# Kernel tuning notes

Measured on AMD Instinct MI355X. Metric: run time of the kernel, lower is better.

## Reference

```python
import jax, jax.numpy as jnp
import numpy as np

N_NODES = 100000
N_EDGES = 1600000
NFEAT, NHID, NCLASS = 512, 128, 40


def setup_inputs() -> dict:
    key = jax.random.key(0)
    ks = jax.random.split(key, 8)
    features = jax.random.normal(ks[0], (N_NODES, NFEAT), dtype=jnp.float32)
    edge_src = jax.random.randint(ks[1], (N_EDGES,), 0, N_NODES, dtype=jnp.int32)
    edge_dst = jax.random.randint(ks[2], (N_EDGES,), 0, N_NODES, dtype=jnp.int32)
    edge_weight = jax.random.uniform(ks[3], (N_EDGES,), dtype=jnp.float32)
    W1 = jax.random.normal(ks[4], (NFEAT, NHID), dtype=jnp.float32) * (1.0 / np.sqrt(NFEAT))
    b1 = jnp.zeros((NHID,), dtype=jnp.float32)
    W2 = jax.random.normal(ks[5], (NHID, NCLASS), dtype=jnp.float32) * (1.0 / np.sqrt(NHID))
    b2 = jnp.zeros((NCLASS,), dtype=jnp.float32)
    return {"features": features, "edge_src": edge_src, "edge_dst": edge_dst,
            "edge_weight": edge_weight, "W1": W1, "b1": b1, "W2": W2, "b2": b2}


def _gcn_conv(x, W, b, edge_src, edge_dst, edge_weight, num_nodes):
    # GCNconv: adj @ (x @ W) + b, adj given as weighted edge list (spmm).
    h = x @ W                                   # [N, out]
    msgs = edge_weight[:, None] * h[edge_src]   # [E, out] gather + scale
    agg = jax.ops.segment_sum(msgs, edge_dst, num_segments=num_nodes)  # [N, out]
    return agg + b


def reference(features, edge_src, edge_dst, edge_weight, W1, b1, W2, b2):
    x = _gcn_conv(features, W1, b1, edge_src, edge_dst, edge_weight, N_NODES)
    x = jax.nn.relu(x)
    # dropout is identity in eval mode (deterministic reference)
    x = _gcn_conv(x, W2, b2, edge_src, edge_dst, edge_weight, N_NODES)
    return jax.nn.log_softmax(x, axis=1)
```

## Files before the change

### kernel.cpp

```cpp
#include <hip/hip_runtime.h>
#include <hip/hip_bf16.h>
#include <math.h>

#define N_NODES 100000
#define N_EDGES 1600000
#define NFEAT 512
#define NHID 128
#define NCLASS 40

#define SCAN_TILE 1024
#define SCAN_NB ((N_NODES + SCAN_TILE - 1) / SCAN_TILE)

#define BSH 8
#define BNODES (1 << BSH)
#define NBUCK ((N_NODES + BNODES - 1) / BNODES)

#define PCHUNK 4096
#define PEPT 16
#define PNB ((N_EDGES + PCHUNK - 1) / PCHUNK)

typedef short bf16x8 __attribute__((ext_vector_type(8)));
typedef float f32x4 __attribute__((ext_vector_type(4)));

static __device__ __forceinline__ unsigned short f32_to_bf16(float f) {
    unsigned int u = __float_as_uint(f);
    unsigned int r = u + 0x7FFFu + ((u >> 16) & 1u);
    return (unsigned short)(r >> 16);
}
static __device__ __forceinline__ float bf16_to_f32(unsigned short h) {
    return __uint_as_float(((unsigned int)h) << 16);
}

__global__ __launch_bounds__(256) void transpose_w1_kernel(
    const float* __restrict__ W1, unsigned short* __restrict__ Wt)
{
    int tid = blockIdx.x * 256 + threadIdx.x;
    int n = tid >> 9;
    int k = tid & 511;
    Wt[tid] = f32_to_bf16(W1[k * NHID + n]);
}

__global__ __launch_bounds__(256) void gemm1_mfma_kernel(
    const float* __restrict__ A,
    const unsigned short* __restrict__ Wt,
    unsigned short* __restrict__ h1b,
    int M)
{
    __shared__ unsigned short cstage[4][32 * 130];

    const int tid = threadIdx.x;
    const int w = tid >> 6;
    const int lane = tid & 63;
    const int lr = lane & 15;
    const int quad = lane >> 4;
    const int m0 = blockIdx.x * 128 + w * 32;

    f32x4 acc[2][8];
    #pragma unroll
    for (int rt = 0; rt < 2; rt++)
        #pragma unroll
        for (int ct = 0; ct < 8; ct++)
            acc[rt][ct] = (f32x4){0.f, 0.f, 0.f, 0.f};

    int r0 = m0 + lr;
    int r1 = m0 + 16 + lr;
    int r0c = r0 < M ? r0 : M - 1;
    int r1c = r1 < M ? r1 : M - 1;
    const float* a0p = A + (size_t)r0c * NFEAT + quad * 8;
    const float* a1p = A + (size_t)r1c * NFEAT + quad * 8;
    const unsigned short* bp = Wt + (size_t)lr * NFEAT + quad * 8;

    #pragma unroll 2
    for (int k0 = 0; k0 < NFEAT; k0 += 32) {
        float4 a0a = *(const float4*)(a0p + k0);
        float4 a0b = *(const float4*)(a0p + k0 + 4);
        float4 a1a = *(const float4*)(a1p + k0);
        float4 a1b = *(const float4*)(a1p + k0 + 4);

        bf16x8 fb[8];
        #pragma unroll
        for (int ct = 0; ct < 8; ct++)
            fb[ct] = *(const bf16x8*)(bp + (size_t)ct * 16 * NFEAT + k0);

        bf16x8 fa0, fa1;
        fa0[0] = (short)f32_to_bf16(a0a.x); fa0[1] = (short)f32_to_bf16(a0a.y);
        fa0[2] = (short)f32_to_bf16(a0a.z); fa0[3] = (short)f32_to_bf16(a0a.w);
        fa0[4] = (short)f32_to_bf16(a0b.x); fa0[5] = (short)f32_to_bf16(a0b.y);
        fa0[6] = (short)f32_to_bf16(a0b.z); fa0[7] = (short)f32_to_bf16(a0b.w);
        fa1[0] = (short)f32_to_bf16(a1a.x); fa1[1] = (short)f32_to_bf16(a1a.y);
        fa1[2] = (short)f32_to_bf16(a1a.z); fa1[3] = (short)f32_to_bf16(a1a.w);
        fa1[4] = (short)f32_to_bf16(a1b.x); fa1[5] = (short)f32_to_bf16(a1b.y);
        fa1[6] = (short)f32_to_bf16(a1b.z); fa1[7] = (short)f32_to_bf16(a1b.w);

        #pragma unroll
        for (int ct = 0; ct < 8; ct++) {
            acc[0][ct] = __builtin_amdgcn_mfma_f32_16x16x32_bf16(fa0, fb[ct], acc[0][ct], 0, 0, 0);
            acc[1][ct] = __builtin_amdgcn_mfma_f32_16x16x32_bf16(fa1, fb[ct], acc[1][ct], 0, 0, 0);
        }
    }

    unsigned short* st = cstage[w];
    #pragma unroll
    for (int rt = 0; rt < 2; rt++)
        #pragma unroll
        for (int ct = 0; ct < 8; ct++)
            #pragma unroll
            for (int i = 0; i < 4; i++) {
                int row = rt * 16 + quad * 4 + i;
                int col = ct * 16 + lr;
                st[row * 130 + col] = f32_to_bf16(acc[rt][ct][i]);
            }

    #pragma unroll
    for (int g = 0; g < 8; g++) {
        int row = g * 4 + (lane >> 4);
        int c8 = lane & 15;
        const unsigned short* rp = &st[row * 130 + c8 * 8];
        uint4 v = *(const uint4*)rp;
        int gr = m0 + row;
        if (gr < M)
            *(uint4*)&h1b[(size_t)gr * NHID + c8 * 8] = v;
    }
}

__global__ __launch_bounds__(256) void hist_kernel(
    const int* __restrict__ dst, int* __restrict__ counts, int E)
{
    int e = blockIdx.x * 256 + threadIdx.x;
    if (e < E) atomicAdd(&counts[dst[e]], 1);
}

__global__ __launch_bounds__(256) void scan_partials_kernel(
    const int* __restrict__ counts, int* __restrict__ partials, int N)
{
    __shared__ int sh[256];
    const int t = threadIdx.x;
    const int base = blockIdx.x * SCAN_TILE + t * 4;
    int s = 0;
    #pragma unroll
    for (int j = 0; j < 4; j++) {
        int i = base + j;
        if (i < N) s += counts[i];
    }
    sh[t] = s;
    __syncthreads();
    #pragma unroll
    for (int off = 128; off > 0; off >>= 1) {
        if (t < off) sh[t] += sh[t + off];
        __syncthreads();
    }
    if (t == 0) partials[blockIdx.x] = sh[0];
}

__global__ __launch_bounds__(128) void scan_offsets_kernel(
    const int* __restrict__ partials, int* __restrict__ bofs,
    int* __restrict__ offsets, int N)
{
    __shared__ int sh[128];
    const int t = threadIdx.x;
    int v = (t < SCAN_NB) ? partials[t] : 0;
    sh[t] = v;
    __syncthreads();
    #pragma unroll
    for (int off = 1; off < 128; off <<= 1) {
        int u = (t >= off) ? sh[t - off] : 0;
        __syncthreads();
        sh[t] += u;
        __syncthreads();
    }
    if (t < SCAN_NB) bofs[t] = sh[t] - v;
    if (t == 127) offsets[N] = sh[127];
}

__global__ __launch_bounds__(256) void scan_final_kernel(
    const int* __restrict__ counts, const int* __restrict__ bofs,
    int* __restrict__ offsets, int N)
{
    __shared__ int sh[256];
    const int t = threadIdx.x;
    const int base = blockIdx.x * SCAN_TILE + t * 4;
    int c[4] = {0, 0, 0, 0};
    #pragma unroll
    for (int j = 0; j < 4; j++) {
        int i = base + j;
        if (i < N) c[j] = counts[i];
    }
    int s = c[0] + c[1] + c[2] + c[3];
    sh[t] = s;
    __syncthreads();
    #pragma unroll
    for (int off = 1; off < 256; off <<= 1) {
        int u = (t >= off) ? sh[t - off] : 0;
        __syncthreads();
        sh[t] += u;
        __syncthreads();
    }
    int run = bofs[blockIdx.x] + sh[t] - s;
    #pragma unroll
    for (int j = 0; j < 4; j++) {
        int i = base + j;
        if (i < N) {
            offsets[i] = run;
            run += c[j];
        }
    }
}

__global__ __launch_bounds__(256) void bucket_init_kernel(
    const int* __restrict__ offsets, int* __restrict__ bcursor, int N)
{
    int b = blockIdx.x * 256 + threadIdx.x;
    if (b < NBUCK) {
        int nb = b << BSH;
        bcursor[b] = offsets[nb < N ? nb : N];
    }
}

__global__ __launch_bounds__(256) void partition_kernel(
    const int* __restrict__ src, const int* __restrict__ dst,
    const float* __restrict__ w, int* __restrict__ bcursor,
    int2* __restrict__ sortedA, int E)
{
    __shared__ int hist[NBUCK];
    __shared__ int bbase[NBUCK];
    const int t = threadIdx.x;
    const int c0 = blockIdx.x * PCHUNK;

    for (int j = t; j < NBUCK; j += 256) hist[j] = 0;
    __syncthreads();

    int  myb[PEPT];
    int2 myv[PEPT];
    #pragma unroll
    for (int i = 0; i < PEPT; i++) {
        int e = c0 + t + i * 256;
        if (e < E) {
            int d = dst[e];
            myb[i] = d >> BSH;
            myv[i] = make_int2(src[e] | ((d & (BNODES - 1)) << 17),
                               __float_as_int(w[e]));
            atomicAdd(&hist[myb[i]], 1);
        } else {
            myb[i] = -1;
        }
    }
    __syncthreads();

    for (int j = t; j < NBUCK; j += 256) {
        int c = hist[j];
        bbase[j] = c ? atomicAdd(&bcursor[j], c) : 0;
    }
    __syncthreads();

    #pragma unroll
    for (int i = 0; i < PEPT; i++) {
        if (myb[i] >= 0) {
            int p = atomicAdd(&bbase[myb[i]], 1);
            sortedA[p] = myv[i];
        }
    }
}

__global__ __launch_bounds__(256) void bucket_sort_kernel(
    const int2* __restrict__ sortedA, const int* __restrict__ offsets,
    int2* __restrict__ sortedB, int N)
{
    __shared__ int lcur[BNODES];
    const int b = blockIdx.x;
    const int t = threadIdx.x;
    const int nb = b << BSH;
    const int nn = min(BNODES, N - nb);
    if (t < nn) lcur[t] = offsets[nb + t];
    __syncthreads();
    const int beg = offsets[nb];
    const int end = offsets[nb + nn < N ? nb + nn : N];
    for (int e = beg + t; e < end; e += 256) {
        int2 v = sortedA[e];
        int dlow = (v.x >> 17) & (BNODES - 1);
        int s = v.x & 0x1FFFF;
        int p = atomicAdd(&lcur[dlow], 1);
        sortedB[p] = make_int2(s, v.y);
    }
}

__global__ __launch_bounds__(256) void seg_agg1_kernel(
    const int2* __restrict__ sorted, const int* __restrict__ offsets,
    const unsigned short* __restrict__ h1b, const float* __restrict__ b1,
    float* __restrict__ x, int N)
{
    const int tid = threadIdx.x;
    const int lane = tid & 31;
    const int node = blockIdx.x * 8 + (tid >> 5);
    if (node >= N) return;
    const int beg = offsets[node];
    const int end = offsets[node + 1];
    float4 acc = {0.f, 0.f, 0.f, 0.f};
    for (int c = beg; c < end; c += 32) {
        int m = end - c;
        if (m > 32) m = 32;
        int s = 0, wb = 0;
        if (lane < m) { int2 sw = sorted[c + lane]; s = sw.x; wb = sw.y; }
        for (int j = 0; j < m; j++) {
            int sj = __shfl(s, j, 32);
            float wj = __int_as_float(__shfl(wb, j, 32));
            ushort4 hv = *(const ushort4*)(h1b + (size_t)sj * NHID + lane * 4);
            acc.x = fmaf(wj, bf16_to_f32(hv.x), acc.x);
            acc.y = fmaf(wj, bf16_to_f32(hv.y), acc.y);
            acc.z = fmaf(wj, bf16_to_f32(hv.z), acc.z);
            acc.w = fmaf(wj, bf16_to_f32(hv.w), acc.w);
        }
    }
    float4 bb = *(const float4*)&b1[lane * 4];
    acc.x = fmaxf(acc.x + bb.x, 0.f);
    acc.y = fmaxf(acc.y + bb.y, 0.f);
    acc.z = fmaxf(acc.z + bb.z, 0.f);
    acc.w = fmaxf(acc.w + bb.w, 0.f);
    *(float4*)&x[(size_t)node * NHID + lane * 4] = acc;
}

__global__ __launch_bounds__(256) void gemm2_kernel(
    const float* __restrict__ x, const float* __restrict__ W2,
    float* __restrict__ h2, int M)
{
    __shared__ float xs[32][128];
    __shared__ float Wt[40][132];

    const int tid = threadIdx.x;
    const int m0 = blockIdx.x * 32;

    #pragma unroll
    for (int i = 0; i < 4; i++) {
        int v = tid + i * 256;
        int row = v >> 5;
        int c4 = (v & 31) * 4;
        *(float4*)&xs[row][c4] = *(const float4*)&x[(size_t)(m0 + row) * NHID + c4];
    }
    #pragma unroll
    for (int i = 0; i < 20; i++) {
        int v = tid + i * 256;
        int k = v / 40;
        int c = v - k * 40;
        Wt[c][k] = W2[v];
    }
    __syncthreads();

    #pragma unroll
    for (int i = 0; i < 5; i++) {
        int o = tid + i * 256;
        int row = o / 40;
        int col = o - row * 40;
        float s = 0.f;
        #pragma unroll
        for (int k4 = 0; k4 < 32; k4++) {
            float4 x4 = *(float4*)&xs[row][k4 * 4];
            float4 w4 = *(float4*)&Wt[col][k4 * 4];
            s = fmaf(x4.x, w4.x, s);
            s = fmaf(x4.y, w4.y, s);
            s = fmaf(x4.z, w4.z, s);
            s = fmaf(x4.w, w4.w, s);
        }
        h2[(size_t)(m0 + row) * NCLASS + col] = s;
    }
}

__global__ __launch_bounds__(256) void seg_agg2_kernel(
    const int2* __restrict__ sorted, const int* __restrict__ offsets,
    const float* __restrict__ h2, const float* __restrict__ b2,
    float* __restrict__ out, int N)
{
    const int tid = threadIdx.x;
    const int lane = tid & 15;
    const int node = blockIdx.x * 16 + (tid >> 4);
    if (node >= N) return;
    const int beg = offsets[node];
    const int end = offsets[node + 1];
    float4 acc = {0.f, 0.f, 0.f, 0.f};
    for (int c = beg; c < end; c += 16) {
        int m = end - c;
        if (m > 16) m = 16;
        int s = 0, wb = 0;
        if (lane < m) { int2 sw = sorted[c + lane]; s = sw.x; wb = sw.y; }
        for (int j = 0; j < m; j++) {
            int sj = __shfl(s, j, 16);
            float wj = __int_as_float(__shfl(wb, j, 16));
            if (lane < 10) {
                float4 v = *(const float4*)&h2[(size_t)sj * NCLASS + lane * 4];
                acc.x = fmaf(wj, v.x, acc.x);
                acc.y = fmaf(wj, v.y, acc.y);
                acc.z = fmaf(wj, v.z, acc.z);
                acc.w = fmaf(wj, v.w, acc.w);
            }
        }
    }
    float mx;
    if (lane < 10) {
        float4 bb = *(const float4*)&b2[lane * 4];
        acc.x += bb.x; acc.y += bb.y; acc.z += bb.z; acc.w += bb.w;
        mx = fmaxf(fmaxf(acc.x, acc.y), fmaxf(acc.z, acc.w));
    } else {
        mx = -INFINITY;
    }
    #pragma unroll
    for (int o = 8; o > 0; o >>= 1) mx = fmaxf(mx, __shfl_xor(mx, o, 16));
    float sm = 0.f;
    if (lane < 10)
        sm = expf(acc.x - mx) + expf(acc.y - mx) + expf(acc.z - mx) + expf(acc.w - mx);
    #pragma unroll
    for (int o = 8; o > 0; o >>= 1) sm += __shfl_xor(sm, o, 16);
    if (lane < 10) {
        float l = mx + logf(sm);
        float4 o4 = {acc.x - l, acc.y - l, acc.z - l, acc.w - l};
        *(float4*)&out[(size_t)node * NCLASS + lane * 4] = o4;
    }
}

extern "C" void kernel_launch(void* const* d_in, const int* in_sizes, int n_in,
                              void* d_out, int out_size, void* d_ws, size_t ws_size,
                              hipStream_t stream) {
    const float* features = (const float*)d_in[0];
    const int* edge_src   = (const int*)d_in[1];
    const int* edge_dst   = (const int*)d_in[2];
    const float* edge_w   = (const float*)d_in[3];
    const float* W1       = (const float*)d_in[4];
    const float* b1       = (const float*)d_in[5];
    const float* W2       = (const float*)d_in[6];
    const float* b2       = (const float*)d_in[7];
    float* out = (float*)d_out;

    char* base = (char*)d_ws;
    float*          x        = (float*)base;
    unsigned short* h1b      = (unsigned short*)(base + 51200000);
    unsigned short* Wt       = (unsigned short*)(base + 76800000);
    int2*           sortedB  = (int2*)(base + 76931072);
    int*            offsets  = (int*)(base + 89731072);
    int*            counts   = (int*)(base + 90131080);
    int*            partials = (int*)(base + 90531080);
    int*            bofs     = (int*)(base + 90531472);
    int*            bcursor  = (int*)(base + 90532000);
    int2*           sortedA  = (int2*)(base + 90540000);
    float*          h2       = (float*)h1b;

    hipMemsetAsync(counts, 0, N_NODES * sizeof(int), stream);

    hist_kernel<<<(N_EDGES + 255) / 256, 256, 0, stream>>>(edge_dst, counts, N_EDGES);
    scan_partials_kernel<<<SCAN_NB, 256, 0, stream>>>(counts, partials, N_NODES);
    scan_offsets_kernel<<<1, 128, 0, stream>>>(partials, bofs, offsets, N_NODES);
    scan_final_kernel<<<SCAN_NB, 256, 0, stream>>>(counts, bofs, offsets, N_NODES);
    bucket_init_kernel<<<(NBUCK + 255) / 256, 256, 0, stream>>>(offsets, bcursor, N_NODES);
    partition_kernel<<<PNB, 256, 0, stream>>>(
        edge_src, edge_dst, edge_w, bcursor, sortedA, N_EDGES);
    bucket_sort_kernel<<<NBUCK, 256, 0, stream>>>(sortedA, offsets, sortedB, N_NODES);

    transpose_w1_kernel<<<(NFEAT * NHID) / 256, 256, 0, stream>>>(W1, Wt);
    gemm1_mfma_kernel<<<(N_NODES + 127) / 128, 256, 0, stream>>>(features, Wt, h1b, N_NODES);

    seg_agg1_kernel<<<(N_NODES + 7) / 8, 256, 0, stream>>>(
        sortedB, offsets, h1b, b1, x, N_NODES);

    gemm2_kernel<<<(N_NODES + 31) / 32, 256, 0, stream>>>(x, W2, h2, N_NODES);

    seg_agg2_kernel<<<(N_NODES + 15) / 16, 256, 0, stream>>>(
        sortedB, offsets, h2, b2, out, N_NODES);
}
```

Measured before the change: 645.4 us.

## Fuse aggregation with second GEMM, merge small kernels, unroll gathers by four

Folds the layer-1 aggregation and the second GEMM into one kernel, so the aggregated hidden features stay in shared memory and are never written to or re-read from global memory. The histogram and W1-transpose kernels become one launch, and the bucket-cursor init moves into the final scan, which removes launches. The edge gather loops in both aggregations are unrolled by four to keep more loads in flight, and the bucket size shrinks from 256 to 128 nodes. The cost is that every 8-node block now reloads W2 into shared memory, which is redundant traffic across 12.5k blocks.

```diff
diff --git a/kernel.cpp b/kernel.cpp
--- a/kernel.cpp
+++ b/kernel.cpp
@@ -11,13 +11,15 @@
 #define SCAN_TILE 1024
 #define SCAN_NB ((N_NODES + SCAN_TILE - 1) / SCAN_TILE)
 
-#define BSH 8
+#define BSH 7
 #define BNODES (1 << BSH)
 #define NBUCK ((N_NODES + BNODES - 1) / BNODES)
 
 #define PCHUNK 4096
 #define PEPT 16
 #define PNB ((N_EDGES + PCHUNK - 1) / PCHUNK)
+
+#define HIST_NB ((N_EDGES + 255) / 256)
 
 typedef short bf16x8 __attribute__((ext_vector_type(8)));
 typedef float f32x4 __attribute__((ext_vector_type(4)));
@@ -31,13 +33,20 @@
     return __uint_as_float(((unsigned int)h) << 16);
 }
 
-__global__ __launch_bounds__(256) void transpose_w1_kernel(
-    const float* __restrict__ W1, unsigned short* __restrict__ Wt)
-{
-    int tid = blockIdx.x * 256 + threadIdx.x;
-    int n = tid >> 9;
-    int k = tid & 511;
-    Wt[tid] = f32_to_bf16(W1[k * NHID + n]);
+__global__ __launch_bounds__(256) void hist_transpose_kernel(
+    const int* __restrict__ dst, int* __restrict__ counts,
+    const float* __restrict__ W1, unsigned short* __restrict__ Wt, int E)
+{
+    int b = blockIdx.x;
+    if (b < HIST_NB) {
+        int e = b * 256 + threadIdx.x;
+        if (e < E) atomicAdd(&counts[dst[e]], 1);
+    } else {
+        int tid = (b - HIST_NB) * 256 + threadIdx.x;
+        int n = tid >> 9;
+        int k = tid & 511;
+        Wt[tid] = f32_to_bf16(W1[k * NHID + n]);
+    }
 }
 
 __global__ __launch_bounds__(256) void gemm1_mfma_kernel(
@@ -123,13 +132,6 @@
     }
 }
 
-__global__ __launch_bounds__(256) void hist_kernel(
-    const int* __restrict__ dst, int* __restrict__ counts, int E)
-{
-    int e = blockIdx.x * 256 + threadIdx.x;
-    if (e < E) atomicAdd(&counts[dst[e]], 1);
-}
-
 __global__ __launch_bounds__(256) void scan_partials_kernel(
     const int* __restrict__ counts, int* __restrict__ partials, int N)
 {
@@ -174,7 +176,7 @@
 
 __global__ __launch_bounds__(256) void scan_final_kernel(
     const int* __restrict__ counts, const int* __restrict__ bofs,
-    int* __restrict__ offsets, int N)
+    int* __restrict__ offsets, int* __restrict__ bcursor, int N)
 {
     __shared__ int sh[256];
     const int t = threadIdx.x;
@@ -201,18 +203,9 @@
         int i = base + j;
         if (i < N) {
             offsets[i] = run;
+            if ((i & (BNODES - 1)) == 0) bcursor[i >> BSH] = run;
             run += c[j];
         }
-    }
-}
-
-__global__ __launch_bounds__(256) void bucket_init_kernel(
-    const int* __restrict__ offsets, int* __restrict__ bcursor, int N)
-{
-    int b = blockIdx.x * 256 + threadIdx.x;
-    if (b < NBUCK) {
-        int nb = b << BSH;
-        bcursor[b] = offsets[nb < N ? nb : N];
     }
 }
 
@@ -283,58 +276,20 @@
     }
 }
 
-__global__ __launch_bounds__(256) void seg_agg1_kernel(
+__global__ __launch_bounds__(256) void seg_agg1_gemm2_kernel(
     const int2* __restrict__ sorted, const int* __restrict__ offsets,
     const unsigned short* __restrict__ h1b, const float* __restrict__ b1,
-    float* __restrict__ x, int N)
-{
+    const float* __restrict__ W2, float* __restrict__ h2, int N)
+{
+    __shared__ float xs[8][128];
+    __shared__ float Wt[40][132];
+
     const int tid = threadIdx.x;
     const int lane = tid & 31;
-    const int node = blockIdx.x * 8 + (tid >> 5);
-    if (node >= N) return;
-    const int beg = offsets[node];
-    const int end = offsets[node + 1];
-    float4 acc = {0.f, 0.f, 0.f, 0.f};
-    for (int c = beg; c < end; c += 32) {
-        int m = end - c;
-        if (m > 32) m = 32;
-        int s = 0, wb = 0;
-        if (lane < m) { int2 sw = sorted[c + lane]; s = sw.x; wb = sw.y; }
-        for (int j = 0; j < m; j++) {
-            int sj = __shfl(s, j, 32);
-            float wj = __int_as_float(__shfl(wb, j, 32));
-            ushort4 hv = *(const ushort4*)(h1b + (size_t)sj * NHID + lane * 4);
-            acc.x = fmaf(wj, bf16_to_f32(hv.x), acc.x);
-            acc.y = fmaf(wj, bf16_to_f32(hv.y), acc.y);
-            acc.z = fmaf(wj, bf16_to_f32(hv.z), acc.z);
-            acc.w = fmaf(wj, bf16_to_f32(hv.w), acc.w);
-        }
-    }
-    float4 bb = *(const float4*)&b1[lane * 4];
-    acc.x = fmaxf(acc.x + bb.x, 0.f);
-    acc.y = fmaxf(acc.y + bb.y, 0.f);
-    acc.z = fmaxf(acc.z + bb.z, 0.f);
-    acc.w = fmaxf(acc.w + bb.w, 0.f);
-    *(float4*)&x[(size_t)node * NHID + lane * 4] = acc;
-}
-
-__global__ __launch_bounds__(256) void gemm2_kernel(
-    const float* __restrict__ x, const float* __restrict__ W2,
-    float* __restrict__ h2, int M)
-{
-    __shared__ float xs[32][128];
-    __shared__ float Wt[40][132];
-
-    const int tid = threadIdx.x;
-    const int m0 = blockIdx.x * 32;
-
-    #pragma unroll
-    for (int i = 0; i < 4; i++) {
-        int v = tid + i * 256;
-        int row = v >> 5;
-        int c4 = (v & 31) * 4;
-        *(float4*)&xs[row][c4] = *(const float4*)&x[(size_t)(m0 + row) * NHID + c4];
-    }
+    const int g = tid >> 5;
+    const int node0 = blockIdx.x * 8;
+    const int node = node0 + g;
+
     #pragma unroll
     for (int i = 0; i < 20; i++) {
         int v = tid + i * 256;
@@ -342,24 +297,86 @@
         int c = v - k * 40;
         Wt[c][k] = W2[v];
     }
-    __syncthreads();
-
-    #pragma unroll
-    for (int i = 0; i < 5; i++) {
+
+    float4 acc = {0.f, 0.f, 0.f, 0.f};
+    if (node < N) {
+        const int beg = offsets[node];
+        const int end = offsets[node + 1];
+        const unsigned short* hb = h1b + lane * 4;
+        for (int cb = beg; cb < end; cb += 32) {
+            int m = end - cb;
+            if (m > 32) m = 32;
+            int s = 0, wb = 0;
+            if (lane < m) { int2 sw = sorted[cb + lane]; s = sw.x; wb = sw.y; }
+            int j = 0;
+            for (; j + 4 <= m; j += 4) {
+                int s0 = __shfl(s, j, 32),     s1 = __shfl(s, j + 1, 32);
+                int s2 = __shfl(s, j + 2, 32), s3 = __shfl(s, j + 3, 32);
+                float w0 = __int_as_float(__shfl(wb, j, 32));
+                float w1 = __int_as_float(__shfl(wb, j + 1, 32));
+                float w2 = __int_as_float(__shfl(wb, j + 2, 32));
+                float w3 = __int_as_float(__shfl(wb, j + 3, 32));
+                ushort4 hv0 = *(const ushort4*)(hb + (size_t)s0 * NHID);
+                ushort4 hv1 = *(const ushort4*)(hb + (size_t)s1 * NHID);
+                ushort4 hv2 = *(const ushort4*)(hb + (size_t)s2 * NHID);
+                ushort4 hv3 = *(const ushort4*)(hb + (size_t)s3 * NHID);
+                acc.x = fmaf(w0, bf16_to_f32(hv0.x), acc.x);
+                acc.y = fmaf(w0, bf16_to_f32(hv0.y), acc.y);
+                acc.z = fmaf(w0, bf16_to_f32(hv0.z), acc.z);
+                acc.w = fmaf(w0, bf16_to_f32(hv0.w), acc.w);
+                acc.x = fmaf(w1, bf16_to_f32(hv1.x), acc.x);
+                acc.y = fmaf(w1, bf16_to_f32(hv1.y), acc.y);
+                acc.z = fmaf(w1, bf16_to_f32(hv1.z), acc.z);
+                acc.w = fmaf(w1, bf16_to_f32(hv1.w), acc.w);
+                acc.x = fmaf(w2, bf16_to_f32(hv2.x), acc.x);
+                acc.y = fmaf(w2, bf16_to_f32(hv2.y), acc.y);
+                acc.z = fmaf(w2, bf16_to_f32(hv2.z), acc.z);
+                acc.w = fmaf(w2, bf16_to_f32(hv2.w), acc.w);
+                acc.x = fmaf(w3, bf16_to_f32(hv3.x), acc.x);
+                acc.y = fmaf(w3, bf16_to_f32(hv3.y), acc.y);
+                acc.z = fmaf(w3, bf16_to_f32(hv3.z), acc.z);
+                acc.w = fmaf(w3, bf16_to_f32(hv3.w), acc.w);
+            }
+            for (; j < m; j++) {
+                int sj = __shfl(s, j, 32);
+                float wj = __int_as_float(__shfl(wb, j, 32));
+                ushort4 hv = *(const ushort4*)(hb + (size_t)sj * NHID);
+                acc.x = fmaf(wj, bf16_to_f32(hv.x), acc.x);
+                acc.y = fmaf(wj, bf16_to_f32(hv.y), acc.y);
+                acc.z = fmaf(wj, bf16_to_f32(hv.z), acc.z);
+                acc.w = fmaf(wj, bf16_to_f32(hv.w), acc.w);
+            }
+        }
+        float4 bb = *(const float4*)&b1[lane * 4];
+        acc.x = fmaxf(acc.x + bb.x, 0.f);
+        acc.y = fmaxf(acc.y + bb.y, 0.f);
+        acc.z = fmaxf(acc.z + bb.z, 0.f);
+        acc.w = fmaxf(acc.w + bb.w, 0.f);
+        *(float4*)&xs[g][lane * 4] = acc;
+    }
+    __syncthreads();
+
+    float* hp = h2 + (size_t)node0 * NCLASS;
+    #pragma unroll
+    for (int i = 0; i < 2; i++) {
         int o = tid + i * 256;
-        int row = o / 40;
-        int col = o - row * 40;
-        float s = 0.f;
-        #pragma unroll
-        for (int k4 = 0; k4 < 32; k4++) {
-            float4 x4 = *(float4*)&xs[row][k4 * 4];
-            float4 w4 = *(float4*)&Wt[col][k4 * 4];
-            s = fmaf(x4.x, w4.x, s);
-            s = fmaf(x4.y, w4.y, s);
-            s = fmaf(x4.z, w4.z, s);
-            s = fmaf(x4.w, w4.w, s);
-        }
-        h2[(size_t)(m0 + row) * NCLASS + col] = s;
+        if (o < 8 * NCLASS) {
+            int row = o / NCLASS;
+            int col = o - row * NCLASS;
+            if (node0 + row < N) {
+                float s = 0.f;
+                #pragma unroll
+                for (int k4 = 0; k4 < 32; k4++) {
+                    float4 x4 = *(float4*)&xs[row][k4 * 4];
+                    float4 w4 = *(float4*)&Wt[col][k4 * 4];
+                    s = fmaf(x4.x, w4.x, s);
+                    s = fmaf(x4.y, w4.y, s);
+                    s = fmaf(x4.z, w4.z, s);
+                    s = fmaf(x4.w, w4.w, s);
+                }
+                hp[o] = s;
+            }
+        }
     }
 }
 
@@ -375,16 +392,40 @@
     const int beg = offsets[node];
     const int end = offsets[node + 1];
     float4 acc = {0.f, 0.f, 0.f, 0.f};
-    for (int c = beg; c < end; c += 16) {
-        int m = end - c;
+    const float* hp = h2 + lane * 4;
+    for (int cb = beg; cb < end; cb += 16) {
+        int m = end - cb;
         if (m > 16) m = 16;
         int s = 0, wb = 0;
-        if (lane < m) { int2 sw = sorted[c + lane]; s = sw.x; wb = sw.y; }
-        for (int j = 0; j < m; j++) {
+        if (lane < m) { int2 sw = sorted[cb + lane]; s = sw.x; wb = sw.y; }
+        int j = 0;
+        for (; j + 4 <= m; j += 4) {
+            int s0 = __shfl(s, j, 16),     s1 = __shfl(s, j + 1, 16);
+            int s2 = __shfl(s, j + 2, 16), s3 = __shfl(s, j + 3, 16);
+            float w0 = __int_as_float(__shfl(wb, j, 16));
+            float w1 = __int_as_float(__shfl(wb, j + 1, 16));
+            float w2 = __int_as_float(__shfl(wb, j + 2, 16));
+            float w3 = __int_as_float(__shfl(wb, j + 3, 16));
+            if (lane < 10) {
+                float4 v0 = *(const float4*)(hp + (size_t)s0 * NCLASS);
+                float4 v1 = *(const float4*)(hp + (size_t)s1 * NCLASS);
+                float4 v2 = *(const float4*)(hp + (size_t)s2 * NCLASS);
+                float4 v3 = *(const float4*)(hp + (size_t)s3 * NCLASS);
+                acc.x = fmaf(w0, v0.x, acc.x); acc.y = fmaf(w0, v0.y, acc.y);
+                acc.z = fmaf(w0, v0.z, acc.z); acc.w = fmaf(w0, v0.w, acc.w);
+                acc.x = fmaf(w1, v1.x, acc.x); acc.y = fmaf(w1, v1.y, acc.y);
+                acc.z = fmaf(w1, v1.z, acc.z); acc.w = fmaf(w1, v1.w, acc.w);
+                acc.x = fmaf(w2, v2.x, acc.x); acc.y = fmaf(w2, v2.y, acc.y);
+                acc.z = fmaf(w2, v2.z, acc.z); acc.w = fmaf(w2, v2.w, acc.w);
+                acc.x = fmaf(w3, v3.x, acc.x); acc.y = fmaf(w3, v3.y, acc.y);
+                acc.z = fmaf(w3, v3.z, acc.z); acc.w = fmaf(w3, v3.w, acc.w);
+            }
+        }
+        for (; j < m; j++) {
             int sj = __shfl(s, j, 16);
             float wj = __int_as_float(__shfl(wb, j, 16));
             if (lane < 10) {
-                float4 v = *(const float4*)&h2[(size_t)sj * NCLASS + lane * 4];
+                float4 v = *(const float4*)(hp + (size_t)sj * NCLASS);
                 acc.x = fmaf(wj, v.x, acc.x);
                 acc.y = fmaf(wj, v.y, acc.y);
                 acc.z = fmaf(wj, v.z, acc.z);
@@ -428,7 +469,7 @@
     float* out = (float*)d_out;
 
     char* base = (char*)d_ws;
-    float*          x        = (float*)base;
+    float*          h2       = (float*)base;
     unsigned short* h1b      = (unsigned short*)(base + 51200000);
     unsigned short* Wt       = (unsigned short*)(base + 76800000);
     int2*           sortedB  = (int2*)(base + 76931072);
@@ -438,26 +479,22 @@
     int*            bofs     = (int*)(base + 90531472);
     int*            bcursor  = (int*)(base + 90532000);
     int2*           sortedA  = (int2*)(base + 90540000);
-    float*          h2       = (float*)h1b;
 
     hipMemsetAsync(counts, 0, N_NODES * sizeof(int), stream);
 
-    hist_kernel<<<(N_EDGES + 255) / 256, 256, 0, stream>>>(edge_dst, counts, N_EDGES);
+    hist_transpose_kernel<<<HIST_NB + (NFEAT * NHID) / 256, 256, 0, stream>>>(
+        edge_dst, counts, W1, Wt, N_EDGES);
     scan_partials_kernel<<<SCAN_NB, 256, 0, stream>>>(counts, partials, N_NODES);
     scan_offsets_kernel<<<1, 128, 0, stream>>>(partials, bofs, offsets, N_NODES);
-    scan_final_kernel<<<SCAN_NB, 256, 0, stream>>>(counts, bofs, offsets, N_NODES);
-    bucket_init_kernel<<<(NBUCK + 255) / 256, 256, 0, stream>>>(offsets, bcursor, N_NODES);
+    scan_final_kernel<<<SCAN_NB, 256, 0, stream>>>(counts, bofs, offsets, bcursor, N_NODES);
     partition_kernel<<<PNB, 256, 0, stream>>>(
         edge_src, edge_dst, edge_w, bcursor, sortedA, N_EDGES);
     bucket_sort_kernel<<<NBUCK, 256, 0, stream>>>(sortedA, offsets, sortedB, N_NODES);
 
-    transpose_w1_kernel<<<(NFEAT * NHID) / 256, 256, 0, stream>>>(W1, Wt);
     gemm1_mfma_kernel<<<(N_NODES + 127) / 128, 256, 0, stream>>>(features, Wt, h1b, N_NODES);
 
-    seg_agg1_kernel<<<(N_NODES + 7) / 8, 256, 0, stream>>>(
-        sortedB, offsets, h1b, b1, x, N_NODES);
-
-    gemm2_kernel<<<(N_NODES + 31) / 32, 256, 0, stream>>>(x, W2, h2, N_NODES);
+    seg_agg1_gemm2_kernel<<<(N_NODES + 7) / 8, 256, 0, stream>>>(
+        sortedB, offsets, h1b, b1, W2, h2, N_NODES);
 
     seg_agg2_kernel<<<(N_NODES + 15) / 16, 256, 0, stream>>>(
         sortedB, offsets, h2, b2, out, N_NODES);
```

After: 600.1 us. 7.0% less time.
